# Kernel tuning notes

Measured on AMD Instinct MI355X. Metric: run time of the kernel, lower is better.

Reference implementation:

```python
import jax, jax.numpy as jnp
import numpy as np

B, C, H, W = 4, 64, 256, 256
HEADS = 4
EPS_LN = 1e-5


def conv2d(x, w, pad, groups=1):
    # x: [B,Cin,H,W], w: [Cout,Cin//groups,kh,kw]
    return jax.lax.conv_general_dilated(
        x, w, window_strides=(1, 1), padding=[(pad, pad), (pad, pad)],
        feature_group_count=groups,
        dimension_numbers=('NCHW', 'OIHW', 'NCHW'))


def layernorm_c(x, w, b):
    # WithBias LayerNorm over channel dim (torch does to_3d -> LN over c -> to_4d)
    mu = jnp.mean(x, axis=1, keepdims=True)
    var = jnp.var(x, axis=1, keepdims=True)
    xn = (x - mu) / jnp.sqrt(var + EPS_LN)
    return xn * w[None, :, None, None] + b[None, :, None, None]


def l2norm(t):
    # torch F.normalize over last dim, eps=1e-12
    n = jnp.linalg.norm(t, axis=-1, keepdims=True)
    return t / jnp.maximum(n, 1e-12)


def setup_inputs() -> dict:
    key = jax.random.key(0)
    ks = jax.random.split(key, 20)
    rn = lambda k, shape, s=0.05: (jax.random.normal(k, shape, jnp.float32) * s)
    return {
        'x':   jax.random.normal(ks[0], (B, C, H, W), jnp.float32),
        'ref': jax.random.normal(ks[1], (B, C, H, W), jnp.float32),
        # LayerNorm params (WithBias)
        'ln1_w': jnp.ones((C,), jnp.float32), 'ln1_b': jnp.zeros((C,), jnp.float32),
        'ln2_w': jnp.ones((C,), jnp.float32), 'ln2_b': jnp.zeros((C,), jnp.float32),
        'ln3_w': jnp.ones((C,), jnp.float32), 'ln3_b': jnp.zeros((C,), jnp.float32),
        # Attention params (bias=False)
        'w_kv':    rn(ks[2], (2 * C, C, 1, 1)),
        'w_kv_dw': rn(ks[3], (2 * C, 1, 3, 3)),
        'w_q':     rn(ks[4], (C, C, 1, 1)),
        'w_q_dw':  rn(ks[5], (C, 1, 3, 3)),
        'w_proj':  rn(ks[6], (C, C, 1, 1)),
        'temperature': jnp.ones((HEADS, 1, 1), jnp.float32),
        # SFM params (bias=False); conv_mul1 is applied twice in the original
        'w_add1': rn(ks[7], (C, C, 3, 3)),
        'w_add2': rn(ks[8], (C, C, 3, 3)),
        'w_mul1': rn(ks[9], (C, C, 3, 3)),
        'w_fuse': rn(ks[10], (C, C, 3, 3)),
    }


def attention(x_kv, x_q, w_kv, w_kv_dw, w_q, w_q_dw, w_proj, temperature):
    b, c, h, w = x_kv.shape
    kv = conv2d(conv2d(x_kv, w_kv, 0), w_kv_dw, 1, groups=2 * c)
    k, v = jnp.split(kv, 2, axis=1)
    q = conv2d(conv2d(x_q, w_q, 0), w_q_dw, 1, groups=c)
    ch = c // HEADS
    resh = lambda t: t.reshape(b, HEADS, ch, h * w)  # b head c (hw)
    q, k, v = l2norm(resh(q)), l2norm(resh(k)), resh(v)
    attn = jnp.einsum('bhcn,bhdn->bhcd', q, k) * temperature[None]  # [b,head,ch,ch]
    attn = jax.nn.softmax(attn, axis=-1)
    out = jnp.einsum('bhcd,bhdn->bhcn', attn, v).reshape(b, c, h, w)
    return conv2d(out, w_proj, 0)


def sfm(x, w_add1, w_add2, w_mul1, w_fuse):
    x_add = conv2d(jax.nn.gelu(conv2d(x, w_add1, 1), approximate=False), w_add2, 1)
    x_mul = conv2d(jax.nn.gelu(conv2d(x, w_mul1, 1), approximate=False), w_mul1, 1)
    x_mul = jax.nn.sigmoid(x_mul)
    return conv2d(x * x_mul + x_add, w_fuse, 1)


def reference(x, ref, ln1_w, ln1_b, ln2_w, ln2_b, ln3_w, ln3_b,
              w_kv, w_kv_dw, w_q, w_q_dw, w_proj, temperature,
              w_add1, w_add2, w_mul1, w_fuse):
    # MyTransformerBlock_FAM.forward(x, ref):
    #   x = x + attn(norm1(ref), norm3(x))  (kv from norm1(ref), q from norm3(x))
    #   x = x + sfm(norm2(x))
    a = attention(layernorm_c(ref, ln1_w, ln1_b), layernorm_c(x, ln3_w, ln3_b),
                  w_kv, w_kv_dw, w_q, w_q_dw, w_proj, temperature)
    x = x + a
    x = x + sfm(layernorm_c(x, ln2_w, ln2_b), w_add1, w_add2, w_mul1, w_fuse)
    return x
```

## Files before the change

kernel.cpp:

```cpp
#include <hip/hip_runtime.h>
#include <math.h>

#define HW 65536
#define NPOS 262144

typedef __attribute__((ext_vector_type(8))) short short8;
typedef __attribute__((ext_vector_type(4))) float float4v;

__device__ __forceinline__ float gelu_exact(float v){
    return 0.5f * v * (1.0f + erff(v * 0.70710678118654752f));
}
__device__ __forceinline__ float sigmoid_(float v){
    return 1.0f / (1.0f + __expf(-v));
}
__device__ __forceinline__ unsigned short f2bf(float f){
    unsigned u = __builtin_bit_cast(unsigned, f);
    unsigned r = (u + 0x7fffu + ((u >> 16) & 1u)) >> 16;
    return (unsigned short)r;
}
__device__ __forceinline__ float bf2f(unsigned short h){
    unsigned u = ((unsigned)h) << 16;
    return __builtin_bit_cast(float, u);
}

__global__ __launch_bounds__(256) void k_wprep(
    const float* __restrict__ w0, const float* __restrict__ w1,
    const float* __restrict__ w2, const float* __restrict__ w3,
    const float* __restrict__ wkv, const float* __restrict__ wq,
    unsigned short* __restrict__ dst,
    unsigned short* __restrict__ whi, unsigned short* __restrict__ wlo)
{
    int gid = blockIdx.x * 256 + threadIdx.x;
    if (gid < 147456){
        int w = gid / 36864;
        int rem = gid - w * 36864;
        int t = rem >> 12;
        int oi = rem & 4095;
        int oc = oi >> 6, ic = oi & 63;
        const float* src = (w == 0) ? w0 : (w == 1) ? w1 : (w == 2) ? w2 : w3;
        dst[gid] = f2bf(src[oc*576 + ic*9 + t]);
    } else {
        int e = gid - 147456;
        int row = e >> 6;
        float f = (row < 128) ? wkv[e] : wq[e - 8192];
        unsigned short h = f2bf(f);
        whi[e] = h;
        wlo[e] = f2bf(f - bf2f(h));
    }
}

__global__ __launch_bounds__(256, 2) void k_ln_1x1_mfma(
    const float* __restrict__ x, const float* __restrict__ ref,
    const float* __restrict__ ln1w, const float* __restrict__ ln1b,
    const float* __restrict__ ln3w, const float* __restrict__ ln3b,
    const unsigned short* __restrict__ whi, const unsigned short* __restrict__ wlo,
    float* __restrict__ kpre, float* __restrict__ vpre, float* __restrict__ qpre,
    float* __restrict__ zbuf)
{
    __shared__ unsigned short Xhi[256*72];
    __shared__ unsigned short Xlo[256*72];
    __shared__ float s_ln[4][64];

    int t = threadIdx.x;
    int b = blockIdx.x >> 8;
    int pos0 = (blockIdx.x & 255) << 8;

    if (blockIdx.x == 0){
        for (int j = t; j < 4608; j += 256) zbuf[j] = 0.f;
    }
    if (t < 64){
        s_ln[0][t] = ln1w[t]; s_ln[1][t] = ln1b[t];
        s_ln[2][t] = ln3w[t]; s_ln[3][t] = ln3b[t];
    }

    int pos = pos0 + t;
    const size_t base = (size_t)b * 64 * HW + pos;
    int wave = t >> 6, lane = t & 63;
    int q = lane >> 4, l = lane & 15;
    int pb = wave * 64;

    {
        float v[64];
        float s = 0.f, ss = 0.f;
        #pragma unroll
        for (int c = 0; c < 64; c++){ float r = ref[base + (size_t)c*HW]; v[c] = r; s += r; ss += r*r; }
        float mu  = s * (1.0f/64.0f);
        float var = ss * (1.0f/64.0f) - mu*mu;
        float inv = rsqrtf(var + 1e-5f);
        __syncthreads();
        #pragma unroll
        for (int c0 = 0; c0 < 64; c0 += 8){
            unsigned short h8[8], l8[8];
            #pragma unroll
            for (int i = 0; i < 8; i++){
                float f = (v[c0+i]-mu)*inv*s_ln[0][c0+i] + s_ln[1][c0+i];
                unsigned short h = f2bf(f);
                h8[i] = h; l8[i] = f2bf(f - bf2f(h));
            }
            *(short8*)(&Xhi[t*72 + c0]) = *(short8*)h8;
            *(short8*)(&Xlo[t*72 + c0]) = *(short8*)l8;
        }
    }
    __syncthreads();

    {
        float4v acc[8][4];
        #pragma unroll
        for (int m = 0; m < 8; m++)
            #pragma unroll
            for (int n = 0; n < 4; n++) acc[m][n] = (float4v){0.f,0.f,0.f,0.f};
        #pragma unroll
        for (int c = 0; c < 2; c++){
            short8 ah[8], al[8];
            #pragma unroll
            for (int m = 0; m < 8; m++){
                ah[m] = *(const short8*)(whi + (m*16 + l)*64 + c*32 + q*8);
                al[m] = *(const short8*)(wlo + (m*16 + l)*64 + c*32 + q*8);
            }
            #pragma unroll
            for (int n = 0; n < 4; n++){
                short8 bh = *(const short8*)(&Xhi[(pb + n*16 + l)*72 + c*32 + q*8]);
                short8 bl = *(const short8*)(&Xlo[(pb + n*16 + l)*72 + c*32 + q*8]);
                #pragma unroll
                for (int m = 0; m < 8; m++){
                    acc[m][n] = __builtin_amdgcn_mfma_f32_16x16x32_bf16(ah[m], bh, acc[m][n], 0, 0, 0);
                    acc[m][n] = __builtin_amdgcn_mfma_f32_16x16x32_bf16(ah[m], bl, acc[m][n], 0, 0, 0);
                    acc[m][n] = __builtin_amdgcn_mfma_f32_16x16x32_bf16(al[m], bh, acc[m][n], 0, 0, 0);
                }
            }
        }
        #pragma unroll
        for (int m = 0; m < 8; m++){
            #pragma unroll
            for (int n = 0; n < 4; n++){
                int px = pos0 + pb + n*16 + l;
                #pragma unroll
                for (int i = 0; i < 4; i++){
                    int oc = m*16 + q*4 + i;
                    float val = acc[m][n][i];
                    if (m < 4) kpre[(size_t)(b*64 + oc)*HW + px] = val;
                    else       vpre[(size_t)(b*64 + (oc-64))*HW + px] = val;
                }
            }
        }
    }
    __syncthreads();

    {
        float v[64];
        float s = 0.f, ss = 0.f;
        #pragma unroll
        for (int c = 0; c < 64; c++){ float r = x[base + (size_t)c*HW]; v[c] = r; s += r; ss += r*r; }
        float mu  = s * (1.0f/64.0f);
        float var = ss * (1.0f/64.0f) - mu*mu;
        float inv = rsqrtf(var + 1e-5f);
        #pragma unroll
        for (int c0 = 0; c0 < 64; c0 += 8){
            unsigned short h8[8], l8[8];
            #pragma unroll
            for (int i = 0; i < 8; i++){
                float f = (v[c0+i]-mu)*inv*s_ln[2][c0+i] + s_ln[3][c0+i];
                unsigned short h = f2bf(f);
                h8[i] = h; l8[i] = f2bf(f - bf2f(h));
            }
            *(short8*)(&Xhi[t*72 + c0]) = *(short8*)h8;
            *(short8*)(&Xlo[t*72 + c0]) = *(short8*)l8;
        }
    }
    __syncthreads();

    {
        float4v acc[4][4];
        #pragma unroll
        for (int m = 0; m < 4; m++)
            #pragma unroll
            for (int n = 0; n < 4; n++) acc[m][n] = (float4v){0.f,0.f,0.f,0.f};
        #pragma unroll
        for (int c = 0; c < 2; c++){
            short8 ah[4], al[4];
            #pragma unroll
            for (int m = 0; m < 4; m++){
                ah[m] = *(const short8*)(whi + (128 + m*16 + l)*64 + c*32 + q*8);
                al[m] = *(const short8*)(wlo + (128 + m*16 + l)*64 + c*32 + q*8);
            }
            #pragma unroll
            for (int n = 0; n < 4; n++){
                short8 bh = *(const short8*)(&Xhi[(pb + n*16 + l)*72 + c*32 + q*8]);
                short8 bl = *(const short8*)(&Xlo[(pb + n*16 + l)*72 + c*32 + q*8]);
                #pragma unroll
                for (int m = 0; m < 4; m++){
                    acc[m][n] = __builtin_amdgcn_mfma_f32_16x16x32_bf16(ah[m], bh, acc[m][n], 0, 0, 0);
                    acc[m][n] = __builtin_amdgcn_mfma_f32_16x16x32_bf16(ah[m], bl, acc[m][n], 0, 0, 0);
                    acc[m][n] = __builtin_amdgcn_mfma_f32_16x16x32_bf16(al[m], bh, acc[m][n], 0, 0, 0);
                }
            }
        }
        #pragma unroll
        for (int m = 0; m < 4; m++){
            #pragma unroll
            for (int n = 0; n < 4; n++){
                int px = pos0 + pb + n*16 + l;
                #pragma unroll
                for (int i = 0; i < 4; i++){
                    int oc = m*16 + q*4 + i;
                    qpre[(size_t)(b*64 + oc)*HW + px] = acc[m][n][i];
                }
            }
        }
    }
}

__global__ __launch_bounds__(256) void k_dw3x3(
    const float* __restrict__ in, const float* __restrict__ w9,
    float* __restrict__ out)
{
    __shared__ float s_in[10*132];
    int t  = threadIdx.x;
    int b  = blockIdx.z >> 6, ch = blockIdx.z & 63;
    int x0 = blockIdx.x * 128, y0 = blockIdx.y * 8;
    const float* src = in + (size_t)(b*64+ch)*HW;
    for (int j = t; j < 1300; j += 256){
        int r = j / 130, cc = j - r*130;
        int gy = y0 - 1 + r, gx = x0 - 1 + cc;
        float val = 0.f;
        if (gy >= 0 && gy < 256 && gx >= 0 && gx < 256) val = src[gy*256 + gx];
        s_in[r*132 + cc] = val;
    }
    float w[9];
    #pragma unroll
    for (int k = 0; k < 9; k++) w[k] = w9[ch*9 + k];
    __syncthreads();
    int ty = t >> 5, tx4 = (t & 31) << 2;
    float o[4] = {0.f, 0.f, 0.f, 0.f};
    #pragma unroll
    for (int ky = 0; ky < 3; ky++){
        float f[6];
        #pragma unroll
        for (int i = 0; i < 6; i++) f[i] = s_in[(ty+ky)*132 + tx4 + i];
        #pragma unroll
        for (int px = 0; px < 4; px++){
            o[px] += w[ky*3+0] * f[px];
            o[px] += w[ky*3+1] * f[px+1];
            o[px] += w[ky*3+2] * f[px+2];
        }
    }
    *(float4v*)(&out[(size_t)(b*64+ch)*HW + (y0+ty)*256 + x0 + tx4]) = *(float4v*)o;
}

__global__ __launch_bounds__(256) void k_qk_mfma(
    const float* __restrict__ q, const float* __restrict__ k,
    float* __restrict__ dots, float* __restrict__ sqq, float* __restrict__ sqk)
{
    int t = threadIdx.x;
    int b = blockIdx.x >> 8;
    int p0 = (blockIdx.x & 255) * 256;
    int wave = t >> 6, lane = t & 63;
    int h = wave;
    int row = lane & 15, kg = lane >> 4;

    const float* qrow = q + (size_t)(b*64 + h*16 + row)*HW;
    const float* krow = k + (size_t)(b*64 + h*16 + row)*HW;

    float4v acc = (float4v){0.f, 0.f, 0.f, 0.f};
    float sq = 0.f, sk = 0.f;

    for (int step = 0; step < 8; step++){
        int p = p0 + step*32 + kg*8;
        float qa[8], ka[8];
        #pragma unroll
        for (int j = 0; j < 8; j++){ qa[j] = qrow[p+j]; ka[j] = krow[p+j]; }
        unsigned short qh8[8], ql8[8], kh8[8], kl8[8];
        #pragma unroll
        for (int j = 0; j < 8; j++){
            sq += qa[j]*qa[j];
            sk += ka[j]*ka[j];
            unsigned short hh = f2bf(qa[j]);
            qh8[j] = hh; ql8[j] = f2bf(qa[j] - bf2f(hh));
            hh = f2bf(ka[j]);
            kh8[j] = hh; kl8[j] = f2bf(ka[j] - bf2f(hh));
        }
        short8 ah = *(short8*)qh8, al = *(short8*)ql8;
        short8 bh = *(short8*)kh8, bl = *(short8*)kl8;
        acc = __builtin_amdgcn_mfma_f32_16x16x32_bf16(ah, bh, acc, 0, 0, 0);
        acc = __builtin_amdgcn_mfma_f32_16x16x32_bf16(ah, bl, acc, 0, 0, 0);
        acc = __builtin_amdgcn_mfma_f32_16x16x32_bf16(al, bh, acc, 0, 0, 0);
    }

    sq += __shfl_xor(sq, 16); sq += __shfl_xor(sq, 32);
    sk += __shfl_xor(sk, 16); sk += __shfl_xor(sk, 32);
    if (lane < 16){
        atomicAdd(&sqq[b*64 + h*16 + row], sq);
        atomicAdd(&sqk[b*64 + h*16 + row], sk);
    }
    int dbase = ((b*4 + h)*16 + kg*4)*16 + row;
    atomicAdd(&dots[dbase + 0*16], acc[0]);
    atomicAdd(&dots[dbase + 1*16], acc[1]);
    atomicAdd(&dots[dbase + 2*16], acc[2]);
    atomicAdd(&dots[dbase + 3*16], acc[3]);
}

__global__ __launch_bounds__(256) void k_softmax_m(
    const float* __restrict__ dots, const float* __restrict__ sqq,
    const float* __restrict__ sqk, const float* __restrict__ temp,
    const float* __restrict__ wproj,
    unsigned short* __restrict__ Mhi, unsigned short* __restrict__ Mlo)
{
    __shared__ float s_wp[4096];
    __shared__ float s_at[1024];
    int t = threadIdx.x;
    int b = blockIdx.x;

    for (int j = t; j < 4096; j += 256) s_wp[j] = wproj[j];

    if (t < 64){
        int h = t >> 4, cq = t & 15;
        float nq = fmaxf(sqrtf(sqq[b*64 + h*16 + cq]), 1e-12f);
        float tp = temp[h];
        float l[16];
        float m = -1e30f;
        #pragma unroll
        for (int d = 0; d < 16; d++){
            float nk = fmaxf(sqrtf(sqk[b*64 + h*16 + d]), 1e-12f);
            float v = dots[((b*4+h)*16 + cq)*16 + d] / (nq*nk) * tp;
            l[d] = v; m = fmaxf(m, v);
        }
        float s = 0.f;
        #pragma unroll
        for (int d = 0; d < 16; d++){ l[d] = __expf(l[d]-m); s += l[d]; }
        float invs = 1.0f / s;
        #pragma unroll
        for (int d = 0; d < 16; d++) s_at[(h*16 + cq)*16 + d] = l[d]*invs;
    }
    __syncthreads();

    for (int e = t; e < 4096; e += 256){
        int c = e >> 6, kk = e & 63;
        int h = kk >> 4, d = kk & 15;
        float a = 0.f;
        #pragma unroll
        for (int r = 0; r < 16; r++)
            a += s_wp[c*64 + h*16 + r] * s_at[(h*16 + r)*16 + d];
        unsigned short hh = f2bf(a);
        Mhi[b*4096 + e] = hh;
        Mlo[b*4096 + e] = f2bf(a - bf2f(hh));
    }
}

__global__ __launch_bounds__(256, 2) void k_attnv_mfma(
    const float* __restrict__ v, const float* __restrict__ x,
    const unsigned short* __restrict__ Mhi_g, const unsigned short* __restrict__ Mlo_g,
    const float* __restrict__ ln2w, const float* __restrict__ ln2b,
    unsigned short* __restrict__ x1_bf, unsigned short* __restrict__ y_bf)
{
    __shared__ unsigned short Mhi[64*72];
    __shared__ unsigned short Mlo[64*72];
    __shared__ float s_lw[64], s_lb[64];
    int t = threadIdx.x;
    int b = blockIdx.x >> 8;
    int pos0 = (blockIdx.x & 255) << 8;

    for (int e = t; e < 4096; e += 256){
        int row = e >> 6, ic = e & 63;
        Mhi[row*72 + ic] = Mhi_g[b*4096 + e];
        Mlo[row*72 + ic] = Mlo_g[b*4096 + e];
    }
    if (t < 64){ s_lw[t] = ln2w[t]; s_lb[t] = ln2b[t]; }
    __syncthreads();

    int wave = t >> 6, lane = t & 63;
    int q = lane >> 4, l = lane & 15;
    int px0 = pos0 + wave*64;

    float4v acc[4][4];
    #pragma unroll
    for (int m = 0; m < 4; m++)
        #pragma unroll
        for (int n = 0; n < 4; n++) acc[m][n] = (float4v){0.f,0.f,0.f,0.f};

    #pragma unroll
    for (int c = 0; c < 2; c++){
        short8 ah[4], al[4];
        #pragma unroll
        for (int m = 0; m < 4; m++){
            ah[m] = *(const short8*)(&Mhi[(m*16 + l)*72 + c*32 + q*8]);
            al[m] = *(const short8*)(&Mlo[(m*16 + l)*72 + c*32 + q*8]);
        }
        #pragma unroll
        for (int n = 0; n < 4; n++){
            float vv[8];
            #pragma unroll
            for (int j = 0; j < 8; j++)
                vv[j] = v[(size_t)(b*64 + c*32 + q*8 + j)*HW + px0 + n*16 + l];
            unsigned short bh8[8], bl8[8];
            #pragma unroll
            for (int j = 0; j < 8; j++){
                unsigned short h = f2bf(vv[j]);
                bh8[j] = h; bl8[j] = f2bf(vv[j] - bf2f(h));
            }
            short8 bh = *(short8*)bh8, bl = *(short8*)bl8;
            #pragma unroll
            for (int m = 0; m < 4; m++){
                acc[m][n] = __builtin_amdgcn_mfma_f32_16x16x32_bf16(ah[m], bh, acc[m][n], 0, 0, 0);
                acc[m][n] = __builtin_amdgcn_mfma_f32_16x16x32_bf16(ah[m], bl, acc[m][n], 0, 0, 0);
                acc[m][n] = __builtin_amdgcn_mfma_f32_16x16x32_bf16(al[m], bh, acc[m][n], 0, 0, 0);
            }
        }
    }

    #pragma unroll
    for (int n = 0; n < 4; n++){
        int px = px0 + n*16 + l;
        float val[4][4];
        float sn = 0.f, ssn = 0.f;
        #pragma unroll
        for (int m = 0; m < 4; m++){
            #pragma unroll
            for (int i = 0; i < 4; i++){
                float f = acc[m][n][i] + x[(size_t)(b*64 + m*16 + q*4 + i)*HW + px];
                val[m][i] = f; sn += f; ssn += f*f;
            }
        }
        sn  += __shfl_xor(sn, 16);  sn  += __shfl_xor(sn, 32);
        ssn += __shfl_xor(ssn, 16); ssn += __shfl_xor(ssn, 32);
        float mu  = sn * (1.0f/64.0f);
        float var = ssn * (1.0f/64.0f) - mu*mu;
        float inv = rsqrtf(var + 1e-5f);
        size_t nb = ((size_t)b*HW + px) * 64;
        #pragma unroll
        for (int m = 0; m < 4; m++){
            int ocb = m*16 + q*4;
            unsigned short xv[4], yv[4];
            #pragma unroll
            for (int i = 0; i < 4; i++){
                float f = val[m][i];
                xv[i] = f2bf(f);
                yv[i] = f2bf((f - mu) * inv * s_lw[ocb+i] + s_lb[ocb+i]);
            }
            *(unsigned long long*)(x1_bf + nb + ocb) = *(unsigned long long*)xv;
            *(unsigned long long*)(y_bf  + nb + ocb) = *(unsigned long long*)yv;
        }
    }
}

template<int MODE>
__global__ __launch_bounds__(256, 3) void k_conv3x3_mfma(
    const unsigned short* __restrict__ in,
    const unsigned short* __restrict__ wt,
    unsigned short* __restrict__ dst,
    const unsigned short* __restrict__ auxA,
    const unsigned short* __restrict__ auxB,
    float* __restrict__ outf)
{
    __shared__ unsigned short Xs[4*130*40];
    __shared__ unsigned short Ws[2][64*40];
    int tid  = threadIdx.x;
    int b    = blockIdx.z;
    int y0   = blockIdx.y * 2;
    int x0   = blockIdx.x * 128;
    int wave = tid >> 6, lane = tid & 63;
    int q = lane >> 4, l = lane & 15;
    int r = wave >> 1;
    int pb = (wave & 1) * 64;

    float4v acc[4][4];
    #pragma unroll
    for (int m = 0; m < 4; m++)
        #pragma unroll
        for (int n = 0; n < 4; n++) acc[m][n] = (float4v){0.f,0.f,0.f,0.f};

    for (int c = 0; c < 2; ++c){
        __syncthreads();
        for (int j = tid; j < 2080; j += 256){
            int row = j / 520;
            int rem = j - row*520;
            int px  = rem >> 2;
            int part= rem & 3;
            int gy = y0 - 1 + row, gx = x0 - 1 + px;
            short8 v = (short8)0;
            if (gy >= 0 && gy < 256 && gx >= 0 && gx < 256){
                v = *(const short8*)(in + (((size_t)b*HW + gy*256 + gx) * 64) + c*32 + part*8);
            }
            *(short8*)(&Xs[(row*130 + px)*40 + part*8]) = v;
        }
        {
            int oc = tid >> 2, part = tid & 3;
            *(short8*)(&Ws[0][oc*40 + part*8]) =
                *(const short8*)(wt + ((size_t)(0*64 + oc))*64 + c*32 + part*8);
        }
        for (int t = 0; t < 9; ++t){
            __syncthreads();
            if (t < 8){
                int oc = tid >> 2, part = tid & 3;
                *(short8*)(&Ws[(t+1)&1][oc*40 + part*8]) =
                    *(const short8*)(wt + ((size_t)((t+1)*64 + oc))*64 + c*32 + part*8);
            }
            int ky = t / 3, kx = t - ky*3;
            const unsigned short* wb = &Ws[t & 1][0];
            short8 afr[4];
            #pragma unroll
            for (int m = 0; m < 4; m++)
                afr[m] = *(const short8*)(wb + (m*16 + l)*40 + q*8);
            #pragma unroll
            for (int n = 0; n < 4; n++){
                int px = pb + n*16 + l;
                short8 bfr = *(const short8*)(&Xs[((r+ky)*130 + px + kx)*40 + q*8]);
                #pragma unroll
                for (int m = 0; m < 4; m++)
                    acc[m][n] = __builtin_amdgcn_mfma_f32_16x16x32_bf16(
                        afr[m], bfr, acc[m][n], 0, 0, 0);
            }
        }
    }

    int gy = y0 + r;
    #pragma unroll
    for (int n = 0; n < 4; n++){
        int gx = x0 + pb + n*16 + l;
        size_t pixbase = ((size_t)b*HW + gy*256 + gx) * 64;
        #pragma unroll
        for (int m = 0; m < 4; m++){
            int ocb = m*16 + q*4;
            float4v av = acc[m][n];
            if (MODE == 0 || MODE == 1){
                unsigned short pk[4];
                #pragma unroll
                for (int i = 0; i < 4; i++){
                    float f = (MODE == 0) ? gelu_exact(av[i]) : av[i];
                    pk[i] = f2bf(f);
                }
                *(unsigned long long*)(dst + pixbase + ocb) = *(unsigned long long*)pk;
            } else if (MODE == 2){
                unsigned long long yu = *(const unsigned long long*)(auxA + pixbase + ocb);
                unsigned long long xu = *(const unsigned long long*)(auxB + pixbase + ocb);
                const unsigned short* y4 = (const unsigned short*)&yu;
                const unsigned short* xa4 = (const unsigned short*)&xu;
                unsigned short pk[4];
                #pragma unroll
                for (int i = 0; i < 4; i++){
                    float z = bf2f(y4[i]) * sigmoid_(av[i]) + bf2f(xa4[i]);
                    pk[i] = f2bf(z);
                }
                *(unsigned long long*)(dst + pixbase + ocb) = *(unsigned long long*)pk;
            } else {
                unsigned long long xu = *(const unsigned long long*)(auxA + pixbase + ocb);
                const unsigned short* x14 = (const unsigned short*)&xu;
                #pragma unroll
                for (int i = 0; i < 4; i++){
                    outf[((size_t)(b*64 + ocb + i))*HW + gy*256 + gx] = bf2f(x14[i]) + av[i];
                }
            }
        }
    }
}

extern "C" void kernel_launch(void* const* d_in, const int* in_sizes, int n_in,
                              void* d_out, int out_size, void* d_ws, size_t ws_size,
                              hipStream_t stream)
{
    const float* x     = (const float*)d_in[0];
    const float* ref   = (const float*)d_in[1];
    const float* ln1w  = (const float*)d_in[2];
    const float* ln1b  = (const float*)d_in[3];
    const float* ln2w  = (const float*)d_in[4];
    const float* ln2b  = (const float*)d_in[5];
    const float* ln3w  = (const float*)d_in[6];
    const float* ln3b  = (const float*)d_in[7];
    const float* wkv   = (const float*)d_in[8];
    const float* wkvdw = (const float*)d_in[9];
    const float* wq    = (const float*)d_in[10];
    const float* wqdw  = (const float*)d_in[11];
    const float* wproj = (const float*)d_in[12];
    const float* temp  = (const float*)d_in[13];
    const float* wadd1 = (const float*)d_in[14];
    const float* wadd2 = (const float*)d_in[15];
    const float* wmul1 = (const float*)d_in[16];
    const float* wfuse = (const float*)d_in[17];
    float* out = (float*)d_out;

    const size_t S = (size_t)4 * 64 * HW;
    float* ws = (float*)d_ws;
    float* b0   = ws;
    float* b1   = ws + S;
    float* b2   = ws + 2*S;
    float* dots = ws + 3*S;
    float* sqq  = dots + 4096;
    float* sqk  = sqq + 256;
    float* attn = sqk + 256;
    unsigned short* Wt   = (unsigned short*)(attn + 4096);
    unsigned short* Mhi  = Wt + 4*36864;
    unsigned short* Mlo  = Mhi + 4*4096;
    unsigned short* WHhi = Mlo + 4*4096;
    unsigned short* WHlo = WHhi + 12288;
    if (ws_size < 3*S*4 + 8704*4 + (4*36864 + 2*4*4096 + 2*12288)*2) return;

    unsigned short* y_bf    = (unsigned short*)b1;
    unsigned short* x1_bf   = (unsigned short*)b1 + S;
    unsigned short* t_bf    = (unsigned short*)b2;
    unsigned short* xadd_bf = (unsigned short*)b2 + S;
    unsigned short* z_bf    = (unsigned short*)b0;

    k_wprep<<<624, 256, 0, stream>>>(wadd1, wadd2, wmul1, wfuse, wkv, wq,
                                     Wt, WHhi, WHlo);

    k_ln_1x1_mfma<<<1024, 256, 0, stream>>>(x, ref, ln1w, ln1b, ln3w, ln3b,
                                            WHhi, WHlo, b0, b1, b2, dots);
    dim3 gdw(2, 32, 256);
    k_dw3x3<<<gdw, 256, 0, stream>>>(b2, wqdw,         out);
    k_dw3x3<<<gdw, 256, 0, stream>>>(b0, wkvdw,        b2);
    k_dw3x3<<<gdw, 256, 0, stream>>>(b1, wkvdw + 64*9, b0);

    k_qk_mfma<<<1024, 256, 0, stream>>>(out, b2, dots, sqq, sqk);
    k_softmax_m<<<4, 256, 0, stream>>>(dots, sqq, sqk, temp, wproj, Mhi, Mlo);

    k_attnv_mfma<<<1024, 256, 0, stream>>>(b0, x, Mhi, Mlo, ln2w, ln2b,
                                           x1_bf, y_bf);

    dim3 gc(2, 128, 4);
    k_conv3x3_mfma<0><<<gc, 256, 0, stream>>>(y_bf, Wt + 0*36864, t_bf,
                                              nullptr, nullptr, nullptr);
    k_conv3x3_mfma<1><<<gc, 256, 0, stream>>>(t_bf, Wt + 1*36864, xadd_bf,
                                              nullptr, nullptr, nullptr);
    k_conv3x3_mfma<0><<<gc, 256, 0, stream>>>(y_bf, Wt + 2*36864, t_bf,
                                              nullptr, nullptr, nullptr);
    k_conv3x3_mfma<2><<<gc, 256, 0, stream>>>(t_bf, Wt + 2*36864, z_bf,
                                              y_bf, xadd_bf, nullptr);
    k_conv3x3_mfma<3><<<gc, 256, 0, stream>>>(z_bf, Wt + 3*36864, nullptr,
                                              x1_bf, nullptr, out);
}
```

Measured before the change: 710.5 us.

## Fuse SFM 3x3 convs sharing inputs into dual-output and dual-input kernels

The two first-stage 3x3 convs (add1 and mul1 on y) now run in one kernel that loads the input tile once and keeps two accumulator sets. The second-stage convs (add2 and mul1 again) are fused into one kernel that accumulates both and applies the sigmoid gating directly, so the intermediate x_add buffer disappears. Five conv launches become three. Weights are now read straight from global memory as MFMA fragments instead of being staged in double-buffered LDS, and launch bounds drop to 2 blocks per SM because of the doubled accumulators. The cost is higher register pressure, lower occupancy, and repeated global weight loads.

```diff
diff --git a/kernel.cpp b/kernel.cpp
--- a/kernel.cpp
+++ b/kernel.cpp
@@ -442,17 +442,14 @@
     }
 }
 
-template<int MODE>
-__global__ __launch_bounds__(256, 3) void k_conv3x3_mfma(
+__global__ __launch_bounds__(256, 2) void k_conv_dual(
     const unsigned short* __restrict__ in,
-    const unsigned short* __restrict__ wt,
-    unsigned short* __restrict__ dst,
-    const unsigned short* __restrict__ auxA,
-    const unsigned short* __restrict__ auxB,
-    float* __restrict__ outf)
+    const unsigned short* __restrict__ wtA,
+    const unsigned short* __restrict__ wtB,
+    unsigned short* __restrict__ o1,
+    unsigned short* __restrict__ o2)
 {
     __shared__ unsigned short Xs[4*130*40];
-    __shared__ unsigned short Ws[2][64*40];
     int tid  = threadIdx.x;
     int b    = blockIdx.z;
     int y0   = blockIdx.y * 2;
@@ -462,11 +459,14 @@
     int r = wave >> 1;
     int pb = (wave & 1) * 64;
 
-    float4v acc[4][4];
+    float4v accA[4][4], accB[4][4];
     #pragma unroll
     for (int m = 0; m < 4; m++)
         #pragma unroll
-        for (int n = 0; n < 4; n++) acc[m][n] = (float4v){0.f,0.f,0.f,0.f};
+        for (int n = 0; n < 4; n++){
+            accA[m][n] = (float4v){0.f,0.f,0.f,0.f};
+            accB[m][n] = (float4v){0.f,0.f,0.f,0.f};
+        }
 
     for (int c = 0; c < 2; ++c){
         __syncthreads();
@@ -482,32 +482,187 @@
             }
             *(short8*)(&Xs[(row*130 + px)*40 + part*8]) = v;
         }
-        {
-            int oc = tid >> 2, part = tid & 3;
-            *(short8*)(&Ws[0][oc*40 + part*8]) =
-                *(const short8*)(wt + ((size_t)(0*64 + oc))*64 + c*32 + part*8);
-        }
+        __syncthreads();
         for (int t = 0; t < 9; ++t){
+            int ky = t / 3, kx = t - ky*3;
+            short8 afrA[4], afrB[4];
+            #pragma unroll
+            for (int m = 0; m < 4; m++){
+                afrA[m] = *(const short8*)(wtA + ((size_t)(t*64 + m*16 + l))*64 + c*32 + q*8);
+                afrB[m] = *(const short8*)(wtB + ((size_t)(t*64 + m*16 + l))*64 + c*32 + q*8);
+            }
+            #pragma unroll
+            for (int n = 0; n < 4; n++){
+                int px = pb + n*16 + l;
+                short8 bfr = *(const short8*)(&Xs[((r+ky)*130 + px + kx)*40 + q*8]);
+                #pragma unroll
+                for (int m = 0; m < 4; m++){
+                    accA[m][n] = __builtin_amdgcn_mfma_f32_16x16x32_bf16(afrA[m], bfr, accA[m][n], 0, 0, 0);
+                    accB[m][n] = __builtin_amdgcn_mfma_f32_16x16x32_bf16(afrB[m], bfr, accB[m][n], 0, 0, 0);
+                }
+            }
+        }
+    }
+
+    int gy = y0 + r;
+    #pragma unroll
+    for (int n = 0; n < 4; n++){
+        int gx = x0 + pb + n*16 + l;
+        size_t pixbase = ((size_t)b*HW + gy*256 + gx) * 64;
+        #pragma unroll
+        for (int m = 0; m < 4; m++){
+            int ocb = m*16 + q*4;
+            unsigned short p1[4], p2[4];
+            #pragma unroll
+            for (int i = 0; i < 4; i++){
+                p1[i] = f2bf(gelu_exact(accA[m][n][i]));
+                p2[i] = f2bf(gelu_exact(accB[m][n][i]));
+            }
+            *(unsigned long long*)(o1 + pixbase + ocb) = *(unsigned long long*)p1;
+            *(unsigned long long*)(o2 + pixbase + ocb) = *(unsigned long long*)p2;
+        }
+    }
+}
+
+__global__ __launch_bounds__(256, 2) void k_conv_zfuse(
+    const unsigned short* __restrict__ in1,
+    const unsigned short* __restrict__ in2,
+    const unsigned short* __restrict__ wtA,
+    const unsigned short* __restrict__ wtB,
+    const unsigned short* __restrict__ yb,
+    unsigned short* __restrict__ zo)
+{
+    __shared__ unsigned short Xs[4*130*40];
+    int tid  = threadIdx.x;
+    int b    = blockIdx.z;
+    int y0   = blockIdx.y * 2;
+    int x0   = blockIdx.x * 128;
+    int wave = tid >> 6, lane = tid & 63;
+    int q = lane >> 4, l = lane & 15;
+    int r = wave >> 1;
+    int pb = (wave & 1) * 64;
+
+    float4v accA[4][4], accB[4][4];
+    #pragma unroll
+    for (int m = 0; m < 4; m++)
+        #pragma unroll
+        for (int n = 0; n < 4; n++){
+            accA[m][n] = (float4v){0.f,0.f,0.f,0.f};
+            accB[m][n] = (float4v){0.f,0.f,0.f,0.f};
+        }
+
+    for (int c = 0; c < 2; ++c){
+        #pragma unroll
+        for (int pass = 0; pass < 2; ++pass){
+            const unsigned short* src = (pass == 0) ? in1 : in2;
+            const unsigned short* wt  = (pass == 0) ? wtA : wtB;
             __syncthreads();
-            if (t < 8){
-                int oc = tid >> 2, part = tid & 3;
-                *(short8*)(&Ws[(t+1)&1][oc*40 + part*8]) =
-                    *(const short8*)(wt + ((size_t)((t+1)*64 + oc))*64 + c*32 + part*8);
-            }
+            for (int j = tid; j < 2080; j += 256){
+                int row = j / 520;
+                int rem = j - row*520;
+                int px  = rem >> 2;
+                int part= rem & 3;
+                int gy = y0 - 1 + row, gx = x0 - 1 + px;
+                short8 v = (short8)0;
+                if (gy >= 0 && gy < 256 && gx >= 0 && gx < 256){
+                    v = *(const short8*)(src + (((size_t)b*HW + gy*256 + gx) * 64) + c*32 + part*8);
+                }
+                *(short8*)(&Xs[(row*130 + px)*40 + part*8]) = v;
+            }
+            __syncthreads();
+            for (int t = 0; t < 9; ++t){
+                int ky = t / 3, kx = t - ky*3;
+                short8 afr[4];
+                #pragma unroll
+                for (int m = 0; m < 4; m++)
+                    afr[m] = *(const short8*)(wt + ((size_t)(t*64 + m*16 + l))*64 + c*32 + q*8);
+                #pragma unroll
+                for (int n = 0; n < 4; n++){
+                    int px = pb + n*16 + l;
+                    short8 bfr = *(const short8*)(&Xs[((r+ky)*130 + px + kx)*40 + q*8]);
+                    #pragma unroll
+                    for (int m = 0; m < 4; m++){
+                        if (pass == 0)
+                            accA[m][n] = __builtin_amdgcn_mfma_f32_16x16x32_bf16(afr[m], bfr, accA[m][n], 0, 0, 0);
+                        else
+                            accB[m][n] = __builtin_amdgcn_mfma_f32_16x16x32_bf16(afr[m], bfr, accB[m][n], 0, 0, 0);
+                    }
+                }
+            }
+        }
+    }
+
+    int gy = y0 + r;
+    #pragma unroll
+    for (int n = 0; n < 4; n++){
+        int gx = x0 + pb + n*16 + l;
+        size_t pixbase = ((size_t)b*HW + gy*256 + gx) * 64;
+        #pragma unroll
+        for (int m = 0; m < 4; m++){
+            int ocb = m*16 + q*4;
+            unsigned long long yu = *(const unsigned long long*)(yb + pixbase + ocb);
+            const unsigned short* y4 = (const unsigned short*)&yu;
+            unsigned short pk[4];
+            #pragma unroll
+            for (int i = 0; i < 4; i++){
+                float z = bf2f(y4[i]) * sigmoid_(accB[m][n][i]) + accA[m][n][i];
+                pk[i] = f2bf(z);
+            }
+            *(unsigned long long*)(zo + pixbase + ocb) = *(unsigned long long*)pk;
+        }
+    }
+}
+
+__global__ __launch_bounds__(256, 2) void k_conv_final(
+    const unsigned short* __restrict__ in,
+    const unsigned short* __restrict__ wt,
+    const unsigned short* __restrict__ x1,
+    float* __restrict__ outf)
+{
+    __shared__ unsigned short Xs[4*130*40];
+    int tid  = threadIdx.x;
+    int b    = blockIdx.z;
+    int y0   = blockIdx.y * 2;
+    int x0   = blockIdx.x * 128;
+    int wave = tid >> 6, lane = tid & 63;
+    int q = lane >> 4, l = lane & 15;
+    int r = wave >> 1;
+    int pb = (wave & 1) * 64;
+
+    float4v acc[4][4];
+    #pragma unroll
+    for (int m = 0; m < 4; m++)
+        #pragma unroll
+        for (int n = 0; n < 4; n++) acc[m][n] = (float4v){0.f,0.f,0.f,0.f};
+
+    for (int c = 0; c < 2; ++c){
+        __syncthreads();
+        for (int j = tid; j < 2080; j += 256){
+            int row = j / 520;
+            int rem = j - row*520;
+            int px  = rem >> 2;
+            int part= rem & 3;
+            int gy = y0 - 1 + row, gx = x0 - 1 + px;
+            short8 v = (short8)0;
+            if (gy >= 0 && gy < 256 && gx >= 0 && gx < 256){
+                v = *(const short8*)(in + (((size_t)b*HW + gy*256 + gx) * 64) + c*32 + part*8);
+            }
+            *(short8*)(&Xs[(row*130 + px)*40 + part*8]) = v;
+        }
+        __syncthreads();
+        for (int t = 0; t < 9; ++t){
             int ky = t / 3, kx = t - ky*3;
-            const unsigned short* wb = &Ws[t & 1][0];
             short8 afr[4];
             #pragma unroll
             for (int m = 0; m < 4; m++)
-                afr[m] = *(const short8*)(wb + (m*16 + l)*40 + q*8);
+                afr[m] = *(const short8*)(wt + ((size_t)(t*64 + m*16 + l))*64 + c*32 + q*8);
             #pragma unroll
             for (int n = 0; n < 4; n++){
                 int px = pb + n*16 + l;
                 short8 bfr = *(const short8*)(&Xs[((r+ky)*130 + px + kx)*40 + q*8]);
                 #pragma unroll
                 for (int m = 0; m < 4; m++)
-                    acc[m][n] = __builtin_amdgcn_mfma_f32_16x16x32_bf16(
-                        afr[m], bfr, acc[m][n], 0, 0, 0);
+                    acc[m][n] = __builtin_amdgcn_mfma_f32_16x16x32_bf16(afr[m], bfr, acc[m][n], 0, 0, 0);
             }
         }
     }
@@ -520,34 +675,11 @@
         #pragma unroll
         for (int m = 0; m < 4; m++){
             int ocb = m*16 + q*4;
-            float4v av = acc[m][n];
-            if (MODE == 0 || MODE == 1){
-                unsigned short pk[4];
-                #pragma unroll
-                for (int i = 0; i < 4; i++){
-                    float f = (MODE == 0) ? gelu_exact(av[i]) : av[i];
-                    pk[i] = f2bf(f);
-                }
-                *(unsigned long long*)(dst + pixbase + ocb) = *(unsigned long long*)pk;
-            } else if (MODE == 2){
-                unsigned long long yu = *(const unsigned long long*)(auxA + pixbase + ocb);
-                unsigned long long xu = *(const unsigned long long*)(auxB + pixbase + ocb);
-                const unsigned short* y4 = (const unsigned short*)&yu;
-                const unsigned short* xa4 = (const unsigned short*)&xu;
-                unsigned short pk[4];
-                #pragma unroll
-                for (int i = 0; i < 4; i++){
-                    float z = bf2f(y4[i]) * sigmoid_(av[i]) + bf2f(xa4[i]);
-                    pk[i] = f2bf(z);
-                }
-                *(unsigned long long*)(dst + pixbase + ocb) = *(unsigned long long*)pk;
-            } else {
-                unsigned long long xu = *(const unsigned long long*)(auxA + pixbase + ocb);
-                const unsigned short* x14 = (const unsigned short*)&xu;
-                #pragma unroll
-                for (int i = 0; i < 4; i++){
-                    outf[((size_t)(b*64 + ocb + i))*HW + gy*256 + gx] = bf2f(x14[i]) + av[i];
-                }
+            unsigned long long xu = *(const unsigned long long*)(x1 + pixbase + ocb);
+            const unsigned short* x14 = (const unsigned short*)&xu;
+            #pragma unroll
+            for (int i = 0; i < 4; i++){
+                outf[((size_t)(b*64 + ocb + i))*HW + gy*256 + gx] = bf2f(x14[i]) + acc[m][n][i];
             }
         }
     }
@@ -593,11 +725,11 @@
     unsigned short* WHlo = WHhi + 12288;
     if (ws_size < 3*S*4 + 8704*4 + (4*36864 + 2*4*4096 + 2*12288)*2) return;
 
-    unsigned short* y_bf    = (unsigned short*)b1;
-    unsigned short* x1_bf   = (unsigned short*)b1 + S;
-    unsigned short* t_bf    = (unsigned short*)b2;
-    unsigned short* xadd_bf = (unsigned short*)b2 + S;
-    unsigned short* z_bf    = (unsigned short*)b0;
+    unsigned short* y_bf  = (unsigned short*)b1;
+    unsigned short* x1_bf = (unsigned short*)b1 + S;
+    unsigned short* t1_bf = (unsigned short*)b2;
+    unsigned short* t2_bf = (unsigned short*)b2 + S;
+    unsigned short* z_bf  = (unsigned short*)b0;
 
     k_wprep<<<624, 256, 0, stream>>>(wadd1, wadd2, wmul1, wfuse, wkv, wq,
                                      Wt, WHhi, WHlo);
@@ -616,14 +748,9 @@
                                            x1_bf, y_bf);
 
     dim3 gc(2, 128, 4);
-    k_conv3x3_mfma<0><<<gc, 256, 0, stream>>>(y_bf, Wt + 0*36864, t_bf,
-                                              nullptr, nullptr, nullptr);
-    k_conv3x3_mfma<1><<<gc, 256, 0, stream>>>(t_bf, Wt + 1*36864, xadd_bf,
-                                              nullptr, nullptr, nullptr);
-    k_conv3x3_mfma<0><<<gc, 256, 0, stream>>>(y_bf, Wt + 2*36864, t_bf,
-                                              nullptr, nullptr, nullptr);
-    k_conv3x3_mfma<2><<<gc, 256, 0, stream>>>(t_bf, Wt + 2*36864, z_bf,
-                                              y_bf, xadd_bf, nullptr);
-    k_conv3x3_mfma<3><<<gc, 256, 0, stream>>>(z_bf, Wt + 3*36864, nullptr,
-                                              x1_bf, nullptr, out);
-}
+    k_conv_dual<<<gc, 256, 0, stream>>>(y_bf, Wt + 0*36864, Wt + 2*36864,
+                                        t1_bf, t2_bf);
+    k_conv_zfuse<<<gc, 256, 0, stream>>>(t1_bf, t2_bf, Wt + 1*36864,
+                                         Wt + 2*36864, y_bf, z_bf);
+    k_conv_final<<<gc, 256, 0, stream>>>(z_bf, Wt + 3*36864, x1_bf, out);
+}
```

After: 801.2 us. 1.13x slower.
